# Kernel optimization log

Measured on AMD Instinct MI355X. Metric: run time of the kernel, lower is better.

Reference implementation:

```python
import jax, jax.numpy as jnp
import numpy as np

EPS = 1e-5  # nn.BatchNorm1d default eps


def setup_inputs() -> dict:
    key = jax.random.key(0)
    k1, k2, k3 = jax.random.split(key, 3)
    B, N, Fin, Fout = 16, 8192, 256, 256
    x = jax.random.normal(k1, (B, N, Fin), dtype=jnp.float32)
    # nn.Linear init: U(-1/sqrt(in), 1/sqrt(in))
    bound = 1.0 / np.sqrt(Fin)
    W = jax.random.uniform(k2, (Fout, Fin), dtype=jnp.float32, minval=-bound, maxval=bound)
    b = jax.random.uniform(k3, (Fout,), dtype=jnp.float32, minval=-bound, maxval=bound)
    gamma = jnp.ones((Fout,), dtype=jnp.float32)   # BatchNorm1d weight
    beta = jnp.zeros((Fout,), dtype=jnp.float32)   # BatchNorm1d bias
    return {"x": x, "W": W, "b": b, "gamma": gamma, "beta": beta}


def reference(x, W, b, gamma, beta):
    # Linear: [B, N, Fin] @ [Fin, Fout] + b -> [B, N, Fout]
    y = jnp.einsum("bnf,of->bno", x, W) + b
    # Per-sample BatchNorm1d (training mode): stats over N (axis=1) per feature,
    # biased variance, shared affine params. Vectorized over the batch loop.
    mean = jnp.mean(y, axis=1, keepdims=True)              # [B, 1, Fout]
    var = jnp.mean((y - mean) ** 2, axis=1, keepdims=True)  # biased var [B, 1, Fout]
    y_hat = (y - mean) * jax.lax.rsqrt(var + EPS)
    return y_hat * gamma + beta
```

## Files before the change

### kernel.cpp

```cpp
#include <hip/hip_runtime.h>
#include <hip/hip_bf16.h>


typedef __attribute__((ext_vector_type(8))) __bf16 bf16x8;
typedef __attribute__((ext_vector_type(4))) float f32x4;
typedef __attribute__((ext_vector_type(8))) unsigned short us8;

#define BDIM   16
#define NDIM   8192
#define FIN    256
#define FOUT   256
#define BM     128
#define BN     128
#define BK     32
#define NTH    256
#define NRBLK  1024
#define NCBLK  2
#define NKS    8
#define TILEB  8192

__device__ __forceinline__ int swz(int r, int c) {
  return r * 64 + ((c ^ (r & 3)) << 4);
}

__device__ __forceinline__ void split8(const float4 v0, const float4 v1,
                                       us8& h, us8& l) {
  float f[8] = {v0.x, v0.y, v0.z, v0.w, v1.x, v1.y, v1.z, v1.w};
#pragma unroll
  for (int i = 0; i < 8; ++i) {
    unsigned int u = __float_as_uint(f[i]);
    h[i] = (unsigned short)(u >> 16);
    float rem = f[i] - __uint_as_float(u & 0xFFFF0000u);
    l[i] = (unsigned short)(__float_as_uint(rem) >> 16);
  }
}

__device__ __forceinline__ void gload_lds16(const void* g, void* l) {
  __builtin_amdgcn_global_load_lds(
      (const __attribute__((address_space(1))) unsigned int*)g,
      (__attribute__((address_space(3))) unsigned int*)l, 16, 0, 0);
}

__global__ void split_x(const float* __restrict__ X,
                        unsigned short* __restrict__ Xh,
                        unsigned short* __restrict__ Xl) {
  const int total = (BDIM * NDIM) * (FIN / 8);
  for (int i = blockIdx.x * blockDim.x + threadIdx.x; i < total;
       i += gridDim.x * blockDim.x) {
    int row = i >> 5;
    int cg  = i & 31;
    int ks = cg >> 2, c = cg & 3;
    const float4* g = (const float4*)(X + (size_t)row * FIN + ks * BK + c * 8);
    float4 v0 = g[0], v1 = g[1];
    us8 h, l;
    split8(v0, v1, h, l);
    size_t tb = ((size_t)(row >> 7) * NKS + ks) * TILEB;
    int boff = swz(row & 127, c);
    *(us8*)((char*)Xh + tb + boff) = h;
    *(us8*)((char*)Xl + tb + boff) = l;
  }
}

__global__ void split_w(const float* __restrict__ W,
                        unsigned short* __restrict__ Wh,
                        unsigned short* __restrict__ Wl) {
  int i = blockIdx.x * blockDim.x + threadIdx.x;
  int row = i >> 5;
  int cg  = i & 31;
  int ks = cg >> 2, c = cg & 3;
  const float4* g = (const float4*)(W + (size_t)row * FIN + ks * BK + c * 8);
  float4 v0 = g[0], v1 = g[1];
  us8 h, l;
  split8(v0, v1, h, l);
  size_t tb = ((size_t)(row >> 7) * NKS + ks) * TILEB;
  int boff = swz(row & 127, c);
  *(us8*)((char*)Wh + tb + boff) = h;
  *(us8*)((char*)Wl + tb + boff) = l;
}

template <int MODE>
__global__ __launch_bounds__(NTH, 4)
void fused_gemm(const unsigned short* __restrict__ Xh,
                const unsigned short* __restrict__ Xl,
                const unsigned short* __restrict__ Wh,
                const unsigned short* __restrict__ Wl,
                float* __restrict__ Y,
                float* __restrict__ P1, float* __restrict__ P2,
                const float* __restrict__ Sc, const float* __restrict__ Tc) {
  __shared__ __align__(16) char lds[4 * TILEB];
  char* Abh = lds;
  char* Abl = lds + TILEB;
  char* Bbh = lds + 2 * TILEB;
  char* Bbl = lds + 3 * TILEB;

  const int tid  = threadIdx.x;
  const int rblk = blockIdx.x;
  const int cblk = blockIdx.y;
  const int wid = tid >> 6, lane = tid & 63;
  const int wr = wid >> 1, wc = wid & 1;
  const int lg = lane >> 4, lr = lane & 15;

  f32x4 acc[4][4];
#pragma unroll
  for (int m = 0; m < 4; ++m)
#pragma unroll
    for (int n = 0; n < 4; ++n) acc[m][n] = f32x4{0.f, 0.f, 0.f, 0.f};

  const char* gAh = (const char*)Xh + (size_t)rblk * NKS * TILEB;
  const char* gAl = (const char*)Xl + (size_t)rblk * NKS * TILEB;
  const char* gBh = (const char*)Wh + (size_t)cblk * NKS * TILEB;
  const char* gBl = (const char*)Wl + (size_t)cblk * NKS * TILEB;

  for (int ks = 0; ks < NKS; ++ks) {
    const size_t kb = (size_t)ks * TILEB;
#pragma unroll
    for (int j = 0; j < 2; ++j) {
      int so = (wid * 2 + j) * 1024;
      int go = so + lane * 16;
      gload_lds16(gAh + kb + go, Abh + so);
      gload_lds16(gAl + kb + go, Abl + so);
      gload_lds16(gBh + kb + go, Bbh + so);
      gload_lds16(gBl + kb + go, Bbl + so);
    }
    __syncthreads();
    bf16x8 ah[4], al[4], bh[4], bl[4];
#pragma unroll
    for (int m = 0; m < 4; ++m) {
      int boff = swz(wr * 64 + m * 16 + lr, lg);
      ah[m] = *(const bf16x8*)(Abh + boff);
      al[m] = *(const bf16x8*)(Abl + boff);
    }
#pragma unroll
    for (int n = 0; n < 4; ++n) {
      int boff = swz(wc * 64 + n * 16 + lr, lg);
      bh[n] = *(const bf16x8*)(Bbh + boff);
      bl[n] = *(const bf16x8*)(Bbl + boff);
    }
#pragma unroll
    for (int m = 0; m < 4; ++m)
#pragma unroll
      for (int n = 0; n < 4; ++n) {
        acc[m][n] = __builtin_amdgcn_mfma_f32_16x16x32_bf16(ah[m], bh[n], acc[m][n], 0, 0, 0);
        acc[m][n] = __builtin_amdgcn_mfma_f32_16x16x32_bf16(ah[m], bl[n], acc[m][n], 0, 0, 0);
        acc[m][n] = __builtin_amdgcn_mfma_f32_16x16x32_bf16(al[m], bh[n], acc[m][n], 0, 0, 0);
      }
    __syncthreads();
  }

  const size_t rowBase = (size_t)rblk * BM;
  const int colBase = cblk * BN;

  if (MODE == 0) {
#pragma unroll
    for (int m = 0; m < 4; ++m) {
      size_t row = rowBase + wr * 64 + m * 16 + lg * 4;
#pragma unroll
      for (int n = 0; n < 4; ++n) {
        int col = colBase + wc * 64 + n * 16 + lr;
#pragma unroll
        for (int r = 0; r < 4; ++r)
          Y[(row + r) * (size_t)FOUT + col] = acc[m][n][r];
      }
    }
  }

  if (MODE <= 1) {
    float ps1[4], ps2[4];
#pragma unroll
    for (int n = 0; n < 4; ++n) {
      ps1[n] = 0.f; ps2[n] = 0.f;
#pragma unroll
      for (int m = 0; m < 4; ++m)
#pragma unroll
        for (int r = 0; r < 4; ++r) {
          float v = acc[m][n][r];
          ps1[n] += v; ps2[n] += v * v;
        }
      ps1[n] += __shfl_xor(ps1[n], 16);
      ps1[n] += __shfl_xor(ps1[n], 32);
      ps2[n] += __shfl_xor(ps2[n], 16);
      ps2[n] += __shfl_xor(ps2[n], 32);
    }
    __syncthreads();
    float* red = (float*)lds;
    if (lane < 16) {
#pragma unroll
      for (int n = 0; n < 4; ++n) {
        red[wid * 64 + n * 16 + lr]       = ps1[n];
        red[256 + wid * 64 + n * 16 + lr] = ps2[n];
      }
    }
    __syncthreads();
    if (tid < BN) {
      int wcs = tid >> 6, j = tid & 63;
      float s1 = red[wcs * 64 + j] + red[(2 + wcs) * 64 + j];
      float s2 = red[256 + wcs * 64 + j] + red[256 + (2 + wcs) * 64 + j];
      P1[(size_t)(colBase + tid) * NRBLK + rblk] = s1;
      P2[(size_t)(colBase + tid) * NRBLK + rblk] = s2;
    }
  }

  if (MODE == 2) {
    const int b = rblk >> 6;
#pragma unroll
    for (int n = 0; n < 4; ++n) {
      int col  = colBase + wc * 64 + n * 16 + lr;
      float sc = Sc[b * FOUT + col];
      float tc = Tc[b * FOUT + col];
#pragma unroll
      for (int m = 0; m < 4; ++m) {
        size_t row = rowBase + wr * 64 + m * 16 + lg * 4;
#pragma unroll
        for (int r = 0; r < 4; ++r)
          Y[(row + r) * (size_t)FOUT + col] = fmaf(acc[m][n][r], sc, tc);
      }
    }
  }
}

__global__ void reduce_stats(const float* __restrict__ P1, const float* __restrict__ P2,
                             const float* __restrict__ gamma, const float* __restrict__ beta,
                             float* __restrict__ Sc, float* __restrict__ Tc) {
  int p = blockIdx.x * 4 + (threadIdx.x >> 6);
  int lane = threadIdx.x & 63;
  int b = p >> 8, o = p & 255;
  size_t base = (size_t)o * NRBLK + b * 64;
  float s1 = P1[base + lane];
  float s2 = P2[base + lane];
#pragma unroll
  for (int off = 32; off; off >>= 1) {
    s1 += __shfl_xor(s1, off);
    s2 += __shfl_xor(s2, off);
  }
  if (lane == 0) {
    float mean = s1 * (1.f / (float)NDIM);
    float var  = s2 * (1.f / (float)NDIM) - mean * mean;
    float g    = gamma[o] * rsqrtf(var + 1e-5f);
    Sc[p] = g;
    Tc[p] = beta[o] - mean * g;
  }
}

__global__ void normalize_y(const float4* __restrict__ Yv,
                            const float* __restrict__ Sc, const float* __restrict__ Tc,
                            float4* __restrict__ Ov) {
  const int total = (BDIM * NDIM * FOUT) / 4;
  for (int i = blockIdx.x * blockDim.x + threadIdx.x; i < total;
       i += gridDim.x * blockDim.x) {
    float4 y = Yv[i];
    size_t e = (size_t)i * 4;
    int o = (int)(e & 255);
    int b = (int)(e >> 21);
    const float4 s = *(const float4*)(Sc + b * 256 + o);
    const float4 t = *(const float4*)(Tc + b * 256 + o);
    float4 r;
    r.x = fmaf(y.x, s.x, t.x);
    r.y = fmaf(y.y, s.y, t.y);
    r.z = fmaf(y.z, s.z, t.z);
    r.w = fmaf(y.w, s.w, t.w);
    Ov[i] = r;
  }
}

extern "C" void kernel_launch(void* const* d_in, const int* in_sizes, int n_in,
                              void* d_out, int out_size, void* d_ws, size_t ws_size,
                              hipStream_t stream) {
  const float* X     = (const float*)d_in[0];
  const float* W     = (const float*)d_in[1];
  const float* gamma = (const float*)d_in[3];
  const float* beta  = (const float*)d_in[4];
  float* out = (float*)d_out;
  char* ws = (char*)d_ws;

  const size_t yB  = (size_t)BDIM * NDIM * FOUT * 4;
  const size_t pB  = (size_t)FOUT * NRBLK * 4;
  const size_t scB = 4096 * 4;
  const size_t wB  = (size_t)FOUT * FIN * 2;
  const size_t xB  = (size_t)BDIM * NDIM * FIN * 2;

  const size_t needAp = 2 * pB + 2 * scB + 2 * wB + 2 * xB;
  const size_t needA  = needAp + yB;

  dim3 grid(NRBLK, NCBLK), blk(NTH);
  if (ws_size >= needA) {
    float* Y  = (float*)ws;
    float* P1 = (float*)(ws + yB);
    float* P2 = (float*)(ws + yB + pB);
    float* Sc = (float*)(ws + yB + 2 * pB);
    float* Tc = (float*)(ws + yB + 2 * pB + scB);
    unsigned short* Wh = (unsigned short*)(ws + yB + 2 * pB + 2 * scB);
    unsigned short* Wl = (unsigned short*)(ws + yB + 2 * pB + 2 * scB + wB);
    unsigned short* Xh = (unsigned short*)(ws + yB + 2 * pB + 2 * scB + 2 * wB);
    unsigned short* Xl = (unsigned short*)(ws + yB + 2 * pB + 2 * scB + 2 * wB + xB);
    split_w<<<32, 256, 0, stream>>>(W, Wh, Wl);
    split_x<<<2048, 256, 0, stream>>>(X, Xh, Xl);
    fused_gemm<0><<<grid, blk, 0, stream>>>(Xh, Xl, Wh, Wl, Y, P1, P2, nullptr, nullptr);
    reduce_stats<<<1024, 256, 0, stream>>>(P1, P2, gamma, beta, Sc, Tc);
    normalize_y<<<4096, 256, 0, stream>>>((const float4*)Y, Sc, Tc, (float4*)out);
  } else {
    float* P1 = (float*)ws;
    float* P2 = (float*)(ws + pB);
    float* Sc = (float*)(ws + 2 * pB);
    float* Tc = (float*)(ws + 2 * pB + scB);
    unsigned short* Wh = (unsigned short*)(ws + 2 * pB + 2 * scB);
    unsigned short* Wl = (unsigned short*)(ws + 2 * pB + 2 * scB + wB);
    unsigned short* Xh = (unsigned short*)(ws + 2 * pB + 2 * scB + 2 * wB);
    unsigned short* Xl = (unsigned short*)(ws + 2 * pB + 2 * scB + 2 * wB + xB);
    split_w<<<32, 256, 0, stream>>>(W, Wh, Wl);
    split_x<<<2048, 256, 0, stream>>>(X, Xh, Xl);
    fused_gemm<1><<<grid, blk, 0, stream>>>(Xh, Xl, Wh, Wl, nullptr, P1, P2, nullptr, nullptr);
    reduce_stats<<<1024, 256, 0, stream>>>(P1, P2, gamma, beta, Sc, Tc);
    fused_gemm<2><<<grid, blk, 0, stream>>>(Xh, Xl, Wh, Wl, out, P1, P2, Sc, Tc);
  }
}
```

Measured before the change: 370.8 us.

## Fuse fp32 split of X into GEMM and widen tile to full output width

Drops the separate split_x pass that wrote bf16 hi/lo copies of X to global memory. The GEMM now reads fp32 X directly, splits it in registers and stores it into LDS. The tile becomes 64 rows by all 256 output columns, so each X row is loaded once rather than once per column block, and the per-block stats reduction no longer goes through LDS. The cost is a synchronous register-path load for A instead of async global-to-LDS, a larger W tile in LDS per block, and twice as many partial-sum entries for reduce_stats.

Measured after the change: 325.8 us. 1.14x faster.

```diff
diff --git a/kernel.cpp b/kernel.cpp
--- a/kernel.cpp
+++ b/kernel.cpp
@@ -10,17 +10,17 @@
 #define NDIM   8192
 #define FIN    256
 #define FOUT   256
-#define BM     128
-#define BN     128
+#define BM     64
+#define BN     256
 #define BK     32
 #define NTH    256
-#define NRBLK  1024
-#define NCBLK  2
+#define NRBLK  2048
 #define NKS    8
-#define TILEB  8192
-
-__device__ __forceinline__ int swz(int r, int c) {
-  return r * 64 + ((c ^ (r & 3)) << 4);
+#define RPB    128
+#define WTILEB 16384
+
+__device__ __forceinline__ int swz64(int r, int c) {
+  return r * 64 + ((c ^ ((r >> 1) & 3)) << 4);
 }
 
 __device__ __forceinline__ void split8(const float4 v0, const float4 v1,
@@ -39,26 +39,6 @@
   __builtin_amdgcn_global_load_lds(
       (const __attribute__((address_space(1))) unsigned int*)g,
       (__attribute__((address_space(3))) unsigned int*)l, 16, 0, 0);
-}
-
-__global__ void split_x(const float* __restrict__ X,
-                        unsigned short* __restrict__ Xh,
-                        unsigned short* __restrict__ Xl) {
-  const int total = (BDIM * NDIM) * (FIN / 8);
-  for (int i = blockIdx.x * blockDim.x + threadIdx.x; i < total;
-       i += gridDim.x * blockDim.x) {
-    int row = i >> 5;
-    int cg  = i & 31;
-    int ks = cg >> 2, c = cg & 3;
-    const float4* g = (const float4*)(X + (size_t)row * FIN + ks * BK + c * 8);
-    float4 v0 = g[0], v1 = g[1];
-    us8 h, l;
-    split8(v0, v1, h, l);
-    size_t tb = ((size_t)(row >> 7) * NKS + ks) * TILEB;
-    int boff = swz(row & 127, c);
-    *(us8*)((char*)Xh + tb + boff) = h;
-    *(us8*)((char*)Xl + tb + boff) = l;
-  }
 }
 
 __global__ void split_w(const float* __restrict__ W,
@@ -72,32 +52,29 @@
   float4 v0 = g[0], v1 = g[1];
   us8 h, l;
   split8(v0, v1, h, l);
-  size_t tb = ((size_t)(row >> 7) * NKS + ks) * TILEB;
-  int boff = swz(row & 127, c);
-  *(us8*)((char*)Wh + tb + boff) = h;
-  *(us8*)((char*)Wl + tb + boff) = l;
+  size_t off = (size_t)ks * WTILEB + swz64(row, c);
+  *(us8*)((char*)Wh + off) = h;
+  *(us8*)((char*)Wl + off) = l;
 }
 
 template <int MODE>
 __global__ __launch_bounds__(NTH, 4)
-void fused_gemm(const unsigned short* __restrict__ Xh,
-                const unsigned short* __restrict__ Xl,
+void fused_gemm(const float* __restrict__ X,
                 const unsigned short* __restrict__ Wh,
                 const unsigned short* __restrict__ Wl,
                 float* __restrict__ Y,
                 float* __restrict__ P1, float* __restrict__ P2,
                 const float* __restrict__ Sc, const float* __restrict__ Tc) {
-  __shared__ __align__(16) char lds[4 * TILEB];
+  __shared__ __align__(16) char lds[8192 + 2 * WTILEB];
   char* Abh = lds;
-  char* Abl = lds + TILEB;
-  char* Bbh = lds + 2 * TILEB;
-  char* Bbl = lds + 3 * TILEB;
+  char* Abl = lds + 4096;
+  char* Bbh = lds + 8192;
+  char* Bbl = lds + 8192 + WTILEB;
 
   const int tid  = threadIdx.x;
   const int rblk = blockIdx.x;
-  const int cblk = blockIdx.y;
+  const size_t rowBase = (size_t)rblk * BM;
   const int wid = tid >> 6, lane = tid & 63;
-  const int wr = wid >> 1, wc = wid & 1;
   const int lg = lane >> 4, lr = lane & 15;
 
   f32x4 acc[4][4];
@@ -106,33 +83,37 @@
 #pragma unroll
     for (int n = 0; n < 4; ++n) acc[m][n] = f32x4{0.f, 0.f, 0.f, 0.f};
 
-  const char* gAh = (const char*)Xh + (size_t)rblk * NKS * TILEB;
-  const char* gAl = (const char*)Xl + (size_t)rblk * NKS * TILEB;
-  const char* gBh = (const char*)Wh + (size_t)cblk * NKS * TILEB;
-  const char* gBl = (const char*)Wl + (size_t)cblk * NKS * TILEB;
+  const int ar = tid >> 2, ac = tid & 3;
 
   for (int ks = 0; ks < NKS; ++ks) {
-    const size_t kb = (size_t)ks * TILEB;
-#pragma unroll
-    for (int j = 0; j < 2; ++j) {
-      int so = (wid * 2 + j) * 1024;
-      int go = so + lane * 16;
-      gload_lds16(gAh + kb + go, Abh + so);
-      gload_lds16(gAl + kb + go, Abl + so);
-      gload_lds16(gBh + kb + go, Bbh + so);
-      gload_lds16(gBl + kb + go, Bbl + so);
+#pragma unroll
+    for (int j = 0; j < 4; ++j) {
+      int so = wid * 4096 + j * 1024;
+      int go = ks * WTILEB + so + lane * 16;
+      gload_lds16((const char*)Wh + go, Bbh + so);
+      gload_lds16((const char*)Wl + go, Bbl + so);
+    }
+    {
+      const float4* g =
+          (const float4*)(X + (rowBase + ar) * (size_t)FIN + ks * BK + ac * 8);
+      float4 v0 = g[0], v1 = g[1];
+      us8 h, l;
+      split8(v0, v1, h, l);
+      int boff = swz64(ar, ac);
+      *(us8*)(Abh + boff) = h;
+      *(us8*)(Abl + boff) = l;
     }
     __syncthreads();
     bf16x8 ah[4], al[4], bh[4], bl[4];
 #pragma unroll
     for (int m = 0; m < 4; ++m) {
-      int boff = swz(wr * 64 + m * 16 + lr, lg);
+      int boff = swz64(m * 16 + lr, lg);
       ah[m] = *(const bf16x8*)(Abh + boff);
       al[m] = *(const bf16x8*)(Abl + boff);
     }
 #pragma unroll
     for (int n = 0; n < 4; ++n) {
-      int boff = swz(wc * 64 + n * 16 + lr, lg);
+      int boff = swz64(wid * 64 + n * 16 + lr, lg);
       bh[n] = *(const bf16x8*)(Bbh + boff);
       bl[n] = *(const bf16x8*)(Bbl + boff);
     }
@@ -147,16 +128,13 @@
     __syncthreads();
   }
 
-  const size_t rowBase = (size_t)rblk * BM;
-  const int colBase = cblk * BN;
-
   if (MODE == 0) {
 #pragma unroll
     for (int m = 0; m < 4; ++m) {
-      size_t row = rowBase + wr * 64 + m * 16 + lg * 4;
+      size_t row = rowBase + m * 16 + lg * 4;
 #pragma unroll
       for (int n = 0; n < 4; ++n) {
-        int col = colBase + wc * 64 + n * 16 + lr;
+        int col = wid * 64 + n * 16 + lr;
 #pragma unroll
         for (int r = 0; r < 4; ++r)
           Y[(row + r) * (size_t)FOUT + col] = acc[m][n][r];
@@ -165,51 +143,38 @@
   }
 
   if (MODE <= 1) {
-    float ps1[4], ps2[4];
 #pragma unroll
     for (int n = 0; n < 4; ++n) {
-      ps1[n] = 0.f; ps2[n] = 0.f;
+      float s1 = 0.f, s2 = 0.f;
 #pragma unroll
       for (int m = 0; m < 4; ++m)
 #pragma unroll
         for (int r = 0; r < 4; ++r) {
           float v = acc[m][n][r];
-          ps1[n] += v; ps2[n] += v * v;
+          s1 += v; s2 += v * v;
         }
-      ps1[n] += __shfl_xor(ps1[n], 16);
-      ps1[n] += __shfl_xor(ps1[n], 32);
-      ps2[n] += __shfl_xor(ps2[n], 16);
-      ps2[n] += __shfl_xor(ps2[n], 32);
-    }
-    __syncthreads();
-    float* red = (float*)lds;
-    if (lane < 16) {
-#pragma unroll
-      for (int n = 0; n < 4; ++n) {
-        red[wid * 64 + n * 16 + lr]       = ps1[n];
-        red[256 + wid * 64 + n * 16 + lr] = ps2[n];
-      }
-    }
-    __syncthreads();
-    if (tid < BN) {
-      int wcs = tid >> 6, j = tid & 63;
-      float s1 = red[wcs * 64 + j] + red[(2 + wcs) * 64 + j];
-      float s2 = red[256 + wcs * 64 + j] + red[256 + (2 + wcs) * 64 + j];
-      P1[(size_t)(colBase + tid) * NRBLK + rblk] = s1;
-      P2[(size_t)(colBase + tid) * NRBLK + rblk] = s2;
+      s1 += __shfl_xor(s1, 16);
+      s1 += __shfl_xor(s1, 32);
+      s2 += __shfl_xor(s2, 16);
+      s2 += __shfl_xor(s2, 32);
+      if (lg == 0) {
+        int col = wid * 64 + n * 16 + lr;
+        P1[(size_t)col * NRBLK + rblk] = s1;
+        P2[(size_t)col * NRBLK + rblk] = s2;
+      }
     }
   }
 
   if (MODE == 2) {
-    const int b = rblk >> 6;
+    const int b = rblk >> 7;
 #pragma unroll
     for (int n = 0; n < 4; ++n) {
-      int col  = colBase + wc * 64 + n * 16 + lr;
+      int col  = wid * 64 + n * 16 + lr;
       float sc = Sc[b * FOUT + col];
       float tc = Tc[b * FOUT + col];
 #pragma unroll
       for (int m = 0; m < 4; ++m) {
-        size_t row = rowBase + wr * 64 + m * 16 + lg * 4;
+        size_t row = rowBase + m * 16 + lg * 4;
 #pragma unroll
         for (int r = 0; r < 4; ++r)
           Y[(row + r) * (size_t)FOUT + col] = fmaf(acc[m][n][r], sc, tc);
@@ -224,9 +189,9 @@
   int p = blockIdx.x * 4 + (threadIdx.x >> 6);
   int lane = threadIdx.x & 63;
   int b = p >> 8, o = p & 255;
-  size_t base = (size_t)o * NRBLK + b * 64;
-  float s1 = P1[base + lane];
-  float s2 = P2[base + lane];
+  size_t base = (size_t)o * NRBLK + b * RPB;
+  float s1 = P1[base + lane] + P1[base + 64 + lane];
+  float s2 = P2[base + lane] + P2[base + 64 + lane];
 #pragma unroll
   for (int off = 32; off; off >>= 1) {
     s1 += __shfl_xor(s1, off);
@@ -276,12 +241,11 @@
   const size_t pB  = (size_t)FOUT * NRBLK * 4;
   const size_t scB = 4096 * 4;
   const size_t wB  = (size_t)FOUT * FIN * 2;
-  const size_t xB  = (size_t)BDIM * NDIM * FIN * 2;
-
-  const size_t needAp = 2 * pB + 2 * scB + 2 * wB + 2 * xB;
+
+  const size_t needAp = 2 * pB + 2 * scB + 2 * wB;
   const size_t needA  = needAp + yB;
 
-  dim3 grid(NRBLK, NCBLK), blk(NTH);
+  dim3 grid(NRBLK), blk(NTH);
   if (ws_size >= needA) {
     float* Y  = (float*)ws;
     float* P1 = (float*)(ws + yB);
@@ -290,11 +254,8 @@
     float* Tc = (float*)(ws + yB + 2 * pB + scB);
     unsigned short* Wh = (unsigned short*)(ws + yB + 2 * pB + 2 * scB);
     unsigned short* Wl = (unsigned short*)(ws + yB + 2 * pB + 2 * scB + wB);
-    unsigned short* Xh = (unsigned short*)(ws + yB + 2 * pB + 2 * scB + 2 * wB);
-    unsigned short* Xl = (unsigned short*)(ws + yB + 2 * pB + 2 * scB + 2 * wB + xB);
     split_w<<<32, 256, 0, stream>>>(W, Wh, Wl);
-    split_x<<<2048, 256, 0, stream>>>(X, Xh, Xl);
-    fused_gemm<0><<<grid, blk, 0, stream>>>(Xh, Xl, Wh, Wl, Y, P1, P2, nullptr, nullptr);
+    fused_gemm<0><<<grid, blk, 0, stream>>>(X, Wh, Wl, Y, P1, P2, nullptr, nullptr);
     reduce_stats<<<1024, 256, 0, stream>>>(P1, P2, gamma, beta, Sc, Tc);
     normalize_y<<<4096, 256, 0, stream>>>((const float4*)Y, Sc, Tc, (float4*)out);
   } else {
@@ -304,12 +265,9 @@
     float* Tc = (float*)(ws + 2 * pB + scB);
     unsigned short* Wh = (unsigned short*)(ws + 2 * pB + 2 * scB);
     unsigned short* Wl = (unsigned short*)(ws + 2 * pB + 2 * scB + wB);
-    unsigned short* Xh = (unsigned short*)(ws + 2 * pB + 2 * scB + 2 * wB);
-    unsigned short* Xl = (unsigned short*)(ws + 2 * pB + 2 * scB + 2 * wB + xB);
     split_w<<<32, 256, 0, stream>>>(W, Wh, Wl);
-    split_x<<<2048, 256, 0, stream>>>(X, Xh, Xl);
-    fused_gemm<1><<<grid, blk, 0, stream>>>(Xh, Xl, Wh, Wl, nullptr, P1, P2, nullptr, nullptr);
+    fused_gemm<1><<<grid, blk, 0, stream>>>(X, Wh, Wl, nullptr, P1, P2, nullptr, nullptr);
     reduce_stats<<<1024, 256, 0, stream>>>(P1, P2, gamma, beta, Sc, Tc);
-    fused_gemm<2><<<grid, blk, 0, stream>>>(Xh, Xl, Wh, Wl, out, P1, P2, Sc, Tc);
-  }
-}
+    fused_gemm<2><<<grid, blk, 0, stream>>>(X, Wh, Wl, out, P1, P2, Sc, Tc);
+  }
+}
```
